# Kernel tuning notes

Measured on AMD Instinct MI355X. Metric: run time of the kernel, lower is better.

Reference implementation:

```python
import jax, jax.numpy as jnp
import numpy as np

NUM_CODES = 4096
TEMPERATURE = 1.0
EPS = 1e-08


def setup_inputs() -> dict:
    key = jax.random.key(0)
    k1, k2, k3 = jax.random.split(key, 3)
    B, D, T = 16, 512, 1500
    encoder_stride = 320
    student_features = jax.random.normal(k1, (B, D, T), dtype=jnp.float32)
    codebook = jax.random.normal(k2, (NUM_CODES, D), dtype=jnp.float32)
    lengths = jax.random.randint(k3, (B,), 0, T * encoder_stride, dtype=jnp.int64)
    return {
        "student_features": student_features,
        "codebook": codebook,
        "lengths": lengths,
        "encoder_stride": encoder_stride,
    }


def _length_mask(lengths, T, stride):
    # frame t is valid iff t < floor(length / stride)  -> (B, T) float mask
    n_valid = jnp.minimum(lengths // stride, T)
    return (jnp.arange(T)[None, :] < n_valid[:, None]).astype(jnp.float32)


def reference(student_features, codebook, lengths, encoder_stride):
    B, D, T = student_features.shape
    mask = _length_mask(lengths, T, encoder_stride)            # (B, T)
    z = jnp.transpose(student_features, (0, 2, 1)).reshape(-1, D)  # (N, D), N = B*T
    # Euclidean cdist via ||z||^2 + ||c||^2 - 2 z c^T (same as torch.cdist GEMM path)
    z2 = jnp.sum(z * z, axis=-1, keepdims=True)                # (N, 1)
    c2 = jnp.sum(codebook * codebook, axis=-1)                 # (K,)
    d2 = z2 + c2[None, :] - 2.0 * (z @ codebook.T)             # (N, K)
    distances = jnp.sqrt(jnp.maximum(d2, 1e-12))
    logits = -distances / TEMPERATURE
    probs = jax.nn.softmax(logits, axis=-1)                    # (N, K)
    probs_masked = probs * mask.reshape(-1, 1)
    code_dist = jnp.sum(probs_masked, axis=0)                  # (K,)
    code_dist = code_dist / (jnp.sum(code_dist) + EPS)
    entropy = -jnp.sum(code_dist * jnp.log(code_dist + EPS))
    max_entropy = jnp.log(jnp.float32(NUM_CODES))
    return 1.0 - entropy / max_entropy
```

## Files before the change

kernel.cpp:

```cpp
#include <hip/hip_runtime.h>
#include <hip/hip_bf16.h>

#define NUM_B   16
#define DIM     512
#define TT      1500
#define NROWS   (NUM_B * TT)
#define NCODES  4096
#define ROW_TILES ((NROWS + 127) / 128)
#define NROWS_PAD (ROW_TILES * 128)
#define NSLICE  8
#define SHIFTC  30.0f
#define NBLKX   (NCODES / 128)
#define TBLKS   (NUM_B * 47)
#define CBLKS   (NCODES / 4)
#define NZERO   (NROWS_PAD + NSLICE * NCODES)

typedef __bf16 bf16x8 __attribute__((ext_vector_type(8)));
typedef float  floatx4 __attribute__((ext_vector_type(4)));
typedef unsigned short ushortx8 __attribute__((ext_vector_type(8)));

__device__ __forceinline__ void glds16(const void* g, void* l) {
    __builtin_amdgcn_global_load_lds(
        (__attribute__((address_space(1))) void*)(void*)g,
        (__attribute__((address_space(3))) void*)l, 16, 0, 0);
}

__global__ __launch_bounds__(256) void k_prep(
    const float* __restrict__ sf, const float* __restrict__ cb,
    unsigned short* __restrict__ zbf, unsigned short* __restrict__ cbbf,
    float* __restrict__ z2, float* __restrict__ c2, float* __restrict__ zero0) {
    int id = blockIdx.x, tid = threadIdx.x;
    if (id < TBLKS) {
        __shared__ float tile[32][257];
        int b = id / 47, t0 = (id % 47) * 32;
        int tl = tid & 31, dg = tid >> 5;
        int tr = tid >> 3, dgr = tid & 7;
        int tg = t0 + tr;
        float ssq = 0.f;
        unsigned short* dst = zbf + (size_t)(b * TT + tg) * DIM;
#pragma unroll
        for (int half = 0; half < 2; ++half) {
            int dbase = half * 256;
            if (half) __syncthreads();
            int t = t0 + tl;
            if (t < TT) {
                const float* src = sf + (size_t)(b * DIM + dbase + dg * 32) * TT + t;
#pragma unroll
                for (int k = 0; k < 32; ++k)
                    tile[tl][dg * 32 + k] = src[(size_t)k * TT];
            }
            __syncthreads();
            if (tg < TT) {
#pragma unroll
                for (int seg = 0; seg < 4; ++seg) {
                    int d0 = seg * 64 + dgr * 8;
                    unsigned int h[8];
#pragma unroll
                    for (int i2 = 0; i2 < 8; ++i2) {
                        __hip_bfloat16 hb = __float2bfloat16(tile[tr][d0 + i2]);
                        h[i2] = __builtin_bit_cast(unsigned short, hb);
                        float vb = __bfloat162float(hb);
                        ssq += vb * vb;
                    }
                    uint4 o;
                    o.x = h[0] | (h[1] << 16); o.y = h[2] | (h[3] << 16);
                    o.z = h[4] | (h[5] << 16); o.w = h[6] | (h[7] << 16);
                    *(uint4*)(dst + dbase + d0) = o;
                }
            }
        }
        ssq += __shfl_xor(ssq, 1); ssq += __shfl_xor(ssq, 2); ssq += __shfl_xor(ssq, 4);
        if (dgr == 0 && tg < TT) z2[b * TT + tg] = ssq;
    } else {
        int ci = id - TBLKS;
        int gid = ci * 256 + tid;
        if (gid < NZERO) zero0[gid] = 0.f;
        int k = ci * 4 + (tid >> 6);
        int lane = tid & 63;
        const float4* src = (const float4*)(cb + (size_t)k * DIM + lane * 8);
        float4 a = src[0], b2 = src[1];
        float vals[8] = {a.x, a.y, a.z, a.w, b2.x, b2.y, b2.z, b2.w};
        float s = 0.f;
        unsigned int h[8];
#pragma unroll
        for (int i = 0; i < 8; ++i) {
            __hip_bfloat16 hb = __float2bfloat16(vals[i]);
            h[i] = __builtin_bit_cast(unsigned short, hb);
            float vb = __bfloat162float(hb);
            s += vb * vb;
        }
        uint4 o;
        o.x = h[0] | (h[1] << 16); o.y = h[2] | (h[3] << 16);
        o.z = h[4] | (h[5] << 16); o.w = h[6] | (h[7] << 16);
        *(uint4*)(cbbf + (size_t)k * DIM + lane * 8) = o;
#pragma unroll
        for (int off = 32; off >= 1; off >>= 1) s += __shfl_down(s, off);
        if (lane == 0) c2[k] = s;
    }
}

__global__ __launch_bounds__(256, 2) void k_gemm1(
    const unsigned short* __restrict__ zbf, const unsigned short* __restrict__ cbbf,
    const float* __restrict__ z2, const float* __restrict__ c2,
    const int* __restrict__ lengths, const int* __restrict__ stride_p,
    float* __restrict__ Sg, unsigned short* __restrict__ Eg) {
    __shared__ unsigned short As[128 * 64];
    __shared__ unsigned short Bs[128 * 64];
    __shared__ float z2s[128], c2s[128];
    __shared__ unsigned char vldp[128];
    __shared__ int s_any;
    int tid = threadIdx.x;
    int r0 = blockIdx.y * 128, c0 = blockIdx.x * 128;
    if (tid == 0) s_any = 0;
    __syncthreads();
    if (tid < 128) {
        int n = r0 + tid;
        int valid = 0;
        if (n < NROWS) {
            int b = n / TT, t = n - b * TT;
            int stride = stride_p[0];
            int nv = lengths[b] / stride;
            if (nv > TT) nv = TT;
            valid = (t < nv);
        }
        if (valid) atomicOr(&s_any, 1);
        vldp[tid] = (unsigned char)valid;
        z2s[tid] = z2[r0 + tid];
        c2s[tid] = c2[c0 + tid];
    }
    __syncthreads();
    if (!s_any) return;

    int wave = tid >> 6, lane = tid & 63;
    int l15 = lane & 15, l4 = lane >> 4;
    int wr = (wave >> 1) * 64, wc = (wave & 1) * 64;

    int srow = lane >> 3;
    int scg = (lane & 7) ^ srow;
    const unsigned short* ag = zbf + (size_t)(r0 + wave * 32 + srow) * DIM + scg * 8;
    const unsigned short* bg = cbbf + (size_t)(c0 + wave * 32 + srow) * DIM + scg * 8;
    unsigned short* al = As + (wave * 32) * 64;
    unsigned short* bl = Bs + (wave * 32) * 64;

    floatx4 acc[4][4];
    const floatx4 zero = {0.f, 0.f, 0.f, 0.f};
#pragma unroll
    for (int i = 0; i < 4; ++i)
#pragma unroll
        for (int j = 0; j < 4; ++j) acc[i][j] = zero;

    int sw = l15 & 7;

    for (int kc = 0; kc < 8; ++kc) {
#pragma unroll
        for (int q = 0; q < 4; ++q) {
            glds16(ag + (size_t)q * 8 * DIM + kc * 64, al + q * 8 * 64);
            glds16(bg + (size_t)q * 8 * DIM + kc * 64, bl + q * 8 * 64);
        }
        __syncthreads();
#pragma unroll
        for (int ks = 0; ks < 64; ks += 32) {
            int g = (ks >> 3) + l4;
            int pcg = g ^ sw;
            bf16x8 av[4], bv[4];
#pragma unroll
            for (int i = 0; i < 4; ++i)
                av[i] = __builtin_bit_cast(bf16x8,
                    *(const ushortx8*)&As[(wr + 16 * i + l15) * 64 + pcg * 8]);
#pragma unroll
            for (int j = 0; j < 4; ++j)
                bv[j] = __builtin_bit_cast(bf16x8,
                    *(const ushortx8*)&Bs[(wc + 16 * j + l15) * 64 + pcg * 8]);
#pragma unroll
            for (int i = 0; i < 4; ++i)
#pragma unroll
                for (int j = 0; j < 4; ++j)
                    acc[i][j] = __builtin_amdgcn_mfma_f32_16x16x32_bf16(av[i], bv[j], acc[i][j], 0, 0, 0);
        }
        __syncthreads();
    }

#pragma unroll
    for (int i = 0; i < 4; ++i) {
#pragma unroll
        for (int r = 0; r < 4; ++r) {
            int rl = wr + 16 * i + 4 * l4 + r;
            bool rv = vldp[rl] != 0;
            float z2v = z2s[rl];
            float s = 0.f;
            unsigned short* Ep = Eg + (size_t)(r0 + rl) * NCODES + c0 + wc + l15;
#pragma unroll
            for (int j = 0; j < 4; ++j) {
                int cl = wc + 16 * j + l15;
                float d2 = z2v + c2s[cl] - 2.0f * acc[i][j][r];
                float d = sqrtf(fmaxf(d2, 1e-12f));
                float e = __expf(SHIFTC - d);
                s += e;
                if (rv) Ep[16 * j] = __builtin_bit_cast(unsigned short, __float2bfloat16(e));
            }
            s += __shfl_xor(s, 1); s += __shfl_xor(s, 2);
            s += __shfl_xor(s, 4); s += __shfl_xor(s, 8);
            if (l15 == 0 && rv) atomicAdd(&Sg[r0 + rl], s);
        }
    }
}

__global__ __launch_bounds__(256) void k_scan(
    const unsigned short* __restrict__ Eg, const float* __restrict__ Sg,
    const int* __restrict__ lengths, const int* __restrict__ stride_p,
    float* __restrict__ cdp) {
    __shared__ float rs[32];
    __shared__ int s_any;
    int tid = threadIdx.x;
    int r0 = blockIdx.y * 32;
    if (tid == 0) s_any = 0;
    __syncthreads();
    if (tid < 32) {
        int n = r0 + tid;
        int valid = 0;
        if (n < NROWS) {
            int b = n / TT, t = n - b * TT;
            int nv = lengths[b] / stride_p[0];
            if (nv > TT) nv = TT;
            valid = (t < nv);
        }
        if (valid) atomicOr(&s_any, 1);
        rs[tid] = valid ? 1.0f / Sg[n] : 0.0f;
    }
    __syncthreads();
    if (!s_any) return;

    int col0 = blockIdx.x * 2048 + tid * 8;
    float acc[8] = {0.f, 0.f, 0.f, 0.f, 0.f, 0.f, 0.f, 0.f};
    for (int nn = 0; nn < 32; ++nn) {
        float rn = rs[nn];
        if (rn == 0.f) continue;
        uint4 v = *(const uint4*)(Eg + (size_t)(r0 + nn) * NCODES + col0);
        unsigned int u[4] = {v.x, v.y, v.z, v.w};
#pragma unroll
        for (int q = 0; q < 4; ++q) {
            acc[2 * q]     += rn * __builtin_bit_cast(float, u[q] << 16);
            acc[2 * q + 1] += rn * __builtin_bit_cast(float, u[q] & 0xffff0000u);
        }
    }
    float* outp = cdp + (size_t)(blockIdx.y & (NSLICE - 1)) * NCODES;
#pragma unroll
    for (int t = 0; t < 8; ++t) atomicAdd(&outp[col0 + t], acc[t]);
}

template <int PASS>
__global__ __launch_bounds__(256, 2) void k_gemm(
    const unsigned short* __restrict__ zbf, const unsigned short* __restrict__ cbbf,
    const float* __restrict__ z2, const float* __restrict__ c2,
    const int* __restrict__ lengths, const int* __restrict__ stride_p,
    float* __restrict__ Sg, float* __restrict__ cd) {
    __shared__ unsigned short As[128 * 64];
    __shared__ unsigned short Bs[128 * 64];
    __shared__ float z2s[128], c2s[128], rs[128];
    __shared__ int s_any;
    int tid = threadIdx.x;
    int r0 = blockIdx.y * 128, c0 = blockIdx.x * 128;
    if (tid == 0) s_any = 0;
    __syncthreads();
    if (tid < 128) {
        int n = r0 + tid;
        int valid = 0;
        if (n < NROWS) {
            int b = n / TT, t = n - b * TT;
            int stride = stride_p[0];
            int nv = lengths[b] / stride;
            if (nv > TT) nv = TT;
            valid = (t < nv);
        }
        if (valid) atomicOr(&s_any, 1);
        z2s[tid] = z2[r0 + tid];
        c2s[tid] = c2[c0 + tid];
        if (PASS == 2) rs[tid] = valid ? (1.0f / Sg[r0 + tid]) : 0.0f;
    }
    __syncthreads();
    if (!s_any) return;

    int wave = tid >> 6, lane = tid & 63;
    int l15 = lane & 15, l4 = lane >> 4;
    int wr = (wave >> 1) * 64, wc = (wave & 1) * 64;
    int srow = lane >> 3;
    int scg = (lane & 7) ^ srow;
    const unsigned short* ag = zbf + (size_t)(r0 + wave * 32 + srow) * DIM + scg * 8;
    const unsigned short* bg = cbbf + (size_t)(c0 + wave * 32 + srow) * DIM + scg * 8;
    unsigned short* al = As + (wave * 32) * 64;
    unsigned short* bl = Bs + (wave * 32) * 64;

    floatx4 acc[4][4];
    const floatx4 zero = {0.f, 0.f, 0.f, 0.f};
#pragma unroll
    for (int i = 0; i < 4; ++i)
#pragma unroll
        for (int j = 0; j < 4; ++j) acc[i][j] = zero;
    int sw = l15 & 7;
    for (int kc = 0; kc < 8; ++kc) {
#pragma unroll
        for (int q = 0; q < 4; ++q) {
            glds16(ag + (size_t)q * 8 * DIM + kc * 64, al + q * 8 * 64);
            glds16(bg + (size_t)q * 8 * DIM + kc * 64, bl + q * 8 * 64);
        }
        __syncthreads();
#pragma unroll
        for (int ks = 0; ks < 64; ks += 32) {
            int g = (ks >> 3) + l4;
            int pcg = g ^ sw;
            bf16x8 av[4], bv[4];
#pragma unroll
            for (int i = 0; i < 4; ++i)
                av[i] = __builtin_bit_cast(bf16x8, *(const ushortx8*)&As[(wr + 16 * i + l15) * 64 + pcg * 8]);
#pragma unroll
            for (int j = 0; j < 4; ++j)
                bv[j] = __builtin_bit_cast(bf16x8, *(const ushortx8*)&Bs[(wc + 16 * j + l15) * 64 + pcg * 8]);
#pragma unroll
            for (int i = 0; i < 4; ++i)
#pragma unroll
                for (int j = 0; j < 4; ++j)
                    acc[i][j] = __builtin_amdgcn_mfma_f32_16x16x32_bf16(av[i], bv[j], acc[i][j], 0, 0, 0);
        }
        __syncthreads();
    }
    if (PASS == 1) {
#pragma unroll
        for (int i = 0; i < 4; ++i) {
#pragma unroll
            for (int r = 0; r < 4; ++r) {
                int rl = wr + 16 * i + 4 * l4 + r;
                float z2v = z2s[rl];
                float s = 0.f;
#pragma unroll
                for (int j = 0; j < 4; ++j) {
                    int cl = wc + 16 * j + l15;
                    float d2 = z2v + c2s[cl] - 2.0f * acc[i][j][r];
                    float d = sqrtf(fmaxf(d2, 1e-12f));
                    s += __expf(SHIFTC - d);
                }
                s += __shfl_xor(s, 1); s += __shfl_xor(s, 2);
                s += __shfl_xor(s, 4); s += __shfl_xor(s, 8);
                if (l15 == 0) atomicAdd(&Sg[r0 + rl], s);
            }
        }
    } else {
#pragma unroll
        for (int j = 0; j < 4; ++j) {
            int cl = wc + 16 * j + l15;
            float c2v = c2s[cl];
            float cs = 0.f;
#pragma unroll
            for (int i = 0; i < 4; ++i) {
#pragma unroll
                for (int r = 0; r < 4; ++r) {
                    int rl = wr + 16 * i + 4 * l4 + r;
                    float d2 = z2s[rl] + c2v - 2.0f * acc[i][j][r];
                    float d = sqrtf(fmaxf(d2, 1e-12f));
                    cs += __expf(SHIFTC - d) * rs[rl];
                }
            }
            cs += __shfl_xor(cs, 16); cs += __shfl_xor(cs, 32);
            if (l4 == 0) atomicAdd(&cd[c0 + cl], cs);
        }
    }
}

__global__ __launch_bounds__(1024) void k_final(const float* __restrict__ cdp,
                                                float* __restrict__ out) {
    __shared__ float red[16];
    __shared__ float tot_s;
    int tid = threadIdx.x, lane = tid & 63, wave = tid >> 6;
    float vloc[4];
    float t = 0.f;
#pragma unroll
    for (int q = 0; q < 4; ++q) {
        int i = tid + q * 1024;
        float v = 0.f;
#pragma unroll
        for (int s = 0; s < NSLICE; ++s) v += cdp[(size_t)s * NCODES + i];
        vloc[q] = v;
        t += v;
    }
#pragma unroll
    for (int off = 32; off >= 1; off >>= 1) t += __shfl_down(t, off);
    if (lane == 0) red[wave] = t;
    __syncthreads();
    if (tid == 0) {
        float tt = 0.f;
#pragma unroll
        for (int w = 0; w < 16; ++w) tt += red[w];
        tot_s = tt;
    }
    __syncthreads();
    float inv = 1.0f / (tot_s + 1e-8f);
    float e = 0.f;
#pragma unroll
    for (int q = 0; q < 4; ++q) {
        float p = vloc[q] * inv;
        e += p * __logf(p + 1e-8f);
    }
#pragma unroll
    for (int off = 32; off >= 1; off >>= 1) e += __shfl_down(e, off);
    if (lane == 0) red[wave] = e;
    __syncthreads();
    if (tid == 0) {
        float ee = 0.f;
#pragma unroll
        for (int w = 0; w < 16; ++w) ee += red[w];
        out[0] = 1.0f - (-ee) / __logf((float)NCODES);
    }
}

extern "C" void kernel_launch(void* const* d_in, const int* in_sizes, int n_in,
                              void* d_out, int out_size, void* d_ws, size_t ws_size,
                              hipStream_t stream) {
    const float* sf = (const float*)d_in[0];
    const float* cb = (const float*)d_in[1];
    const int* lengths = (const int*)d_in[2];
    const int* stride_p = (const int*)d_in[3];

    float* wsf = (float*)d_ws;
    float* Sg = wsf;
    float* cdp = Sg + NROWS_PAD;
    const size_t OFF_Z2 = NZERO;
    const size_t OFF_C2 = OFF_Z2 + NROWS_PAD;
    const size_t OFF_ZB = (OFF_C2 + NCODES + 3) & ~(size_t)3;
    float* z2 = wsf + OFF_Z2;
    float* c2 = wsf + OFF_C2;
    unsigned short* zbf = (unsigned short*)(wsf + OFF_ZB);
    unsigned short* cbbf = zbf + (size_t)NROWS_PAD * DIM;
    unsigned short* Eg = cbbf + (size_t)NCODES * DIM;

    size_t need = OFF_ZB * 4
                + ((size_t)NROWS_PAD * DIM + (size_t)NCODES * DIM
                 + (size_t)NROWS_PAD * NCODES) * 2;

    k_prep<<<dim3(TBLKS + CBLKS), 256, 0, stream>>>(sf, cb, zbf, cbbf, z2, c2, Sg);
    if (ws_size >= need) {
        k_gemm1<<<dim3(NBLKX, ROW_TILES), 256, 0, stream>>>(
            zbf, cbbf, z2, c2, lengths, stride_p, Sg, Eg);
        k_scan<<<dim3(2, NROWS_PAD / 32), 256, 0, stream>>>(
            Eg, Sg, lengths, stride_p, cdp);
    } else {
        k_gemm<1><<<dim3(NBLKX, ROW_TILES), 256, 0, stream>>>(zbf, cbbf, z2, c2, lengths, stride_p, Sg, cdp);
        k_gemm<2><<<dim3(NBLKX, ROW_TILES), 256, 0, stream>>>(zbf, cbbf, z2, c2, lengths, stride_p, Sg, cdp);
    }
    k_final<<<1, 1024, 0, stream>>>(cdp, (float*)d_out);
}
```

Baseline: 238.9 us.

## Rewrite distance GEMM with 256x256 tiles and double-buffered software-pipelined LDS

Replaces the 128x128 single-buffered GEMM1 kernel with a 512-thread, 256x256-tile kernel. It double-buffers LDS and interleaves global-to-LDS staging of the next K tiles with MFMA phases, using hand-placed waitcnt and barriers, inline ds_read_b128 and s_setprio. It also swizzles the workgroup order for cache locality and reshapes the epilogue so each lane writes 4 contiguous bf16 values instead of scattered 2-byte stores. The aim is to hide load latency and cut per-tile overhead. The cost is 128KB of LDS per block, which limits occupancy to one block per CU, plus fragile manual synchronisation.

New measurement: 315.1 us. 1.32x slower.

```diff
diff --git a/kernel.cpp b/kernel.cpp
--- a/kernel.cpp
+++ b/kernel.cpp
@@ -15,6 +15,11 @@
 #define CBLKS   (NCODES / 4)
 #define NZERO   (NROWS_PAD + NSLICE * NCODES)
 
+#define NTY2 (NROWS_PAD / 256)
+#define NTX2 (NCODES / 256)
+#define NWG2 (NTY2 * NTX2)
+#define KTILES (DIM / 64)
+
 typedef __bf16 bf16x8 __attribute__((ext_vector_type(8)));
 typedef float  floatx4 __attribute__((ext_vector_type(4)));
 typedef unsigned short ushortx8 __attribute__((ext_vector_type(8)));
@@ -99,15 +104,256 @@
     }
 }
 
-__global__ __launch_bounds__(256, 2) void k_gemm1(
+
+#define DSR(dst, addr) asm volatile("ds_read_b128 %0, %1" : "=v"(dst) : "v"(addr))
+#define PIPE_SYNC() do { \
+    asm volatile("s_waitcnt vmcnt(8)" ::: "memory"); \
+    asm volatile("s_barrier" ::: "memory"); \
+    asm volatile("s_waitcnt lgkmcnt(0)" ::: "memory"); \
+    __builtin_amdgcn_sched_barrier(0); \
+} while (0)
+#define PIPE_POST() asm volatile("s_barrier" ::: "memory")
+
+#define STG_A(TT_, H_) do { \
+    const unsigned short* _s = agp + (size_t)(H_) * 128 * DIM + (TT_) * 64; \
+    unsigned short* _d = &As[(TT_) & 1][H_][0] + (wave << 9); \
+    glds16(_s, _d); glds16(_s + (size_t)64 * DIM, _d + 4096); \
+} while (0)
+#define STG_B(TT_, H_) do { \
+    const unsigned short* _s = bgp + (size_t)(H_) * 128 * DIM + (TT_) * 64; \
+    unsigned short* _d = &Bs[(TT_) & 1][H_][0] + (wave << 9); \
+    glds16(_s, _d); glds16(_s + (size_t)64 * DIM, _d + 4096); \
+} while (0)
+
+#define MFMA_PH(IB, NQ) do { \
+    __builtin_amdgcn_s_setprio(1); \
+    _Pragma("unroll") \
+    for (int ii = 0; ii < 4; ++ii) { \
+        _Pragma("unroll") \
+        for (int jj = 0; jj < 2; ++jj) { \
+            floatx4 c_ = acc[(IB) + ii][(NQ) * 2 + jj]; \
+            c_ = __builtin_amdgcn_mfma_f32_16x16x32_bf16( \
+                __builtin_bit_cast(bf16x8, bv[NQ][jj][0]), \
+                __builtin_bit_cast(bf16x8, av[ii][0]), c_, 0, 0, 0); \
+            c_ = __builtin_amdgcn_mfma_f32_16x16x32_bf16( \
+                __builtin_bit_cast(bf16x8, bv[NQ][jj][1]), \
+                __builtin_bit_cast(bf16x8, av[ii][1]), c_, 0, 0, 0); \
+            acc[(IB) + ii][(NQ) * 2 + jj] = c_; \
+        } \
+    } \
+    __builtin_amdgcn_s_setprio(0); \
+} while (0)
+
+__global__ __launch_bounds__(512, 2) void k_gemm1(
     const unsigned short* __restrict__ zbf, const unsigned short* __restrict__ cbbf,
     const float* __restrict__ z2, const float* __restrict__ c2,
     const int* __restrict__ lengths, const int* __restrict__ stride_p,
     float* __restrict__ Sg, unsigned short* __restrict__ Eg) {
-    __shared__ unsigned short As[128 * 64];
-    __shared__ unsigned short Bs[128 * 64];
-    __shared__ float z2s[128], c2s[128];
-    __shared__ unsigned char vldp[128];
+    __shared__ alignas(16) unsigned short As[2][2][8192];
+    __shared__ alignas(16) unsigned short Bs[2][2][8192];
+    __shared__ float z2s[256], c2s[256];
+    __shared__ unsigned char vldp[256];
+    __shared__ int s_any;
+
+    int tid = threadIdx.x;
+    int wg = blockIdx.x;
+    int swz = (wg & 7) * (NWG2 / 8) + (wg >> 3);
+    int bx = swz & (NTX2 - 1);
+    int by = swz >> 4;
+    int r0 = by * 256, c0 = bx * 256;
+
+    if (tid == 0) s_any = 0;
+    __syncthreads();
+    if (tid < 256) {
+        int n = r0 + tid;
+        int valid = 0;
+        if (n < NROWS) {
+            int b = n / TT, t_ = n - b * TT;
+            int nv = lengths[b] / stride_p[0];
+            if (nv > TT) nv = TT;
+            valid = (t_ < nv);
+        }
+        if (valid) atomicOr(&s_any, 1);
+        vldp[tid] = (unsigned char)valid;
+        z2s[tid] = z2[r0 + tid];
+        c2s[tid] = c2[c0 + tid];
+    }
+    __syncthreads();
+    if (!s_any) return;
+
+    int wave = tid >> 6, lane = tid & 63;
+    int l15 = lane & 15, l4 = lane >> 4;
+    int wr2 = wave >> 2;
+    int wc4 = wave & 3;
+
+    int srow8 = lane >> 3;
+    int sg = (lane & 7) ^ srow8;
+    const unsigned short* agp = zbf + (size_t)(r0 + wave * 8 + srow8) * DIM + sg * 8;
+    const unsigned short* bgp = cbbf + (size_t)(c0 + wave * 8 + srow8) * DIM + sg * 8;
+
+    unsigned AsB = (unsigned)(size_t)&As[0][0][0];
+    unsigned BsB = (unsigned)(size_t)&Bs[0][0][0];
+    unsigned rowA = (unsigned)((wr2 * 16 + l15) * 128);
+    unsigned rowB = (unsigned)((wc4 * 16 + l15) * 128);
+    unsigned p0 = (unsigned)(((l4) ^ (l15 & 7)) * 16);
+    unsigned p1 = (unsigned)(((4 + l4) ^ (l15 & 7)) * 16);
+
+    floatx4 acc[8][4];
+    const floatx4 zacc = {0.f, 0.f, 0.f, 0.f};
+#pragma unroll
+    for (int i = 0; i < 8; ++i)
+#pragma unroll
+        for (int j = 0; j < 4; ++j) acc[i][j] = zacc;
+
+    STG_A(0, 0); STG_B(0, 0); STG_B(0, 1); STG_A(0, 1); STG_A(1, 0); STG_B(1, 0);
+    asm volatile("s_waitcnt vmcnt(8)" ::: "memory");
+    asm volatile("s_barrier" ::: "memory");
+
+#pragma unroll
+    for (int t = 0; t < KTILES; ++t) {
+        unsigned dbase = (unsigned)((t & 1) * 32768);
+        unsigned aAh0 = AsB + dbase + rowA;
+        unsigned aAh1 = aAh0 + 16384u;
+        unsigned aBh0 = BsB + dbase + rowB;
+        unsigned aBh1 = aBh0 + 16384u;
+        ushortx8 av[4][2];
+        ushortx8 bv[2][2][2];
+
+        {
+            unsigned a0 = aAh0 + p0, a1 = aAh0 + p1;
+            DSR(av[0][0], a0); DSR(av[1][0], a0 + 4096u);
+            DSR(av[2][0], a0 + 8192u); DSR(av[3][0], a0 + 12288u);
+            DSR(av[0][1], a1); DSR(av[1][1], a1 + 4096u);
+            DSR(av[2][1], a1 + 8192u); DSR(av[3][1], a1 + 12288u);
+            unsigned b0 = aBh0 + p0, b1 = aBh0 + p1;
+            DSR(bv[0][0][0], b0); DSR(bv[0][1][0], b0 + 8192u);
+            DSR(bv[0][0][1], b1); DSR(bv[0][1][1], b1 + 8192u);
+        }
+        if (t + 1 < KTILES) STG_B(t + 1, 1);
+        PIPE_SYNC();
+        MFMA_PH(0, 0);
+        PIPE_POST();
+
+        {
+            unsigned b0 = aBh1 + p0, b1 = aBh1 + p1;
+            DSR(bv[1][0][0], b0); DSR(bv[1][1][0], b0 + 8192u);
+            DSR(bv[1][0][1], b1); DSR(bv[1][1][1], b1 + 8192u);
+        }
+        if (t + 1 < KTILES) STG_A(t + 1, 1);
+        PIPE_SYNC();
+        MFMA_PH(0, 1);
+        PIPE_POST();
+
+        {
+            unsigned a0 = aAh1 + p0, a1 = aAh1 + p1;
+            DSR(av[0][0], a0); DSR(av[1][0], a0 + 4096u);
+            DSR(av[2][0], a0 + 8192u); DSR(av[3][0], a0 + 12288u);
+            DSR(av[0][1], a1); DSR(av[1][1], a1 + 4096u);
+            DSR(av[2][1], a1 + 8192u); DSR(av[3][1], a1 + 12288u);
+        }
+        if (t + 2 < KTILES) STG_A(t + 2, 0);
+        PIPE_SYNC();
+        MFMA_PH(4, 0);
+        PIPE_POST();
+
+        if (t + 2 < KTILES) STG_B(t + 2, 0);
+        PIPE_SYNC();
+        MFMA_PH(4, 1);
+        PIPE_POST();
+    }
+
+    float c2r[4][4];
+#pragma unroll
+    for (int j = 0; j < 4; ++j)
+#pragma unroll
+        for (int r = 0; r < 4; ++r)
+            c2r[j][r] = c2s[j * 64 + wc4 * 16 + l4 * 4 + r];
+
+#pragma unroll
+    for (int i = 0; i < 8; ++i) {
+        int rl = i * 32 + wr2 * 16 + l15;
+        bool rv = vldp[rl] != 0;
+        float z2v = z2s[rl];
+        float s = 0.f;
+        unsigned short* Ep = Eg + (size_t)(r0 + rl) * NCODES + c0 + wc4 * 16 + l4 * 4;
+#pragma unroll
+        for (int j = 0; j < 4; ++j) {
+            float e[4];
+#pragma unroll
+            for (int r = 0; r < 4; ++r) {
+                float d2 = z2v + c2r[j][r] - 2.0f * acc[i][j][r];
+                float d = sqrtf(fmaxf(d2, 1e-12f));
+                e[r] = __expf(SHIFTC - d);
+                s += e[r];
+            }
+            if (rv) {
+                unsigned h0 = __builtin_bit_cast(unsigned short, __float2bfloat16(e[0]));
+                unsigned h1 = __builtin_bit_cast(unsigned short, __float2bfloat16(e[1]));
+                unsigned h2 = __builtin_bit_cast(unsigned short, __float2bfloat16(e[2]));
+                unsigned h3 = __builtin_bit_cast(unsigned short, __float2bfloat16(e[3]));
+                uint2 o;
+                o.x = h0 | (h1 << 16);
+                o.y = h2 | (h3 << 16);
+                *(uint2*)(Ep + (size_t)j * 64) = o;
+            }
+        }
+        s += __shfl_xor(s, 16); s += __shfl_xor(s, 32);
+        if (l4 == 0 && rv) atomicAdd(&Sg[r0 + rl], s);
+    }
+}
+
+__global__ __launch_bounds__(256) void k_scan(
+    const unsigned short* __restrict__ Eg, const float* __restrict__ Sg,
+    const int* __restrict__ lengths, const int* __restrict__ stride_p,
+    float* __restrict__ cdp) {
+    __shared__ float rs[32];
+    __shared__ int s_any;
+    int tid = threadIdx.x;
+    int r0 = blockIdx.y * 32;
+    if (tid == 0) s_any = 0;
+    __syncthreads();
+    if (tid < 32) {
+        int n = r0 + tid;
+        int valid = 0;
+        if (n < NROWS) {
+            int b = n / TT, t = n - b * TT;
+            int nv = lengths[b] / stride_p[0];
+            if (nv > TT) nv = TT;
+            valid = (t < nv);
+        }
+        if (valid) atomicOr(&s_any, 1);
+        rs[tid] = valid ? 1.0f / Sg[n] : 0.0f;
+    }
+    __syncthreads();
+    if (!s_any) return;
+
+    int col0 = blockIdx.x * 2048 + tid * 8;
+    float acc[8] = {0.f, 0.f, 0.f, 0.f, 0.f, 0.f, 0.f, 0.f};
+    for (int nn = 0; nn < 32; ++nn) {
+        float rn = rs[nn];
+        if (rn == 0.f) continue;
+        uint4 v = *(const uint4*)(Eg + (size_t)(r0 + nn) * NCODES + col0);
+        unsigned int u[4] = {v.x, v.y, v.z, v.w};
+#pragma unroll
+        for (int q = 0; q < 4; ++q) {
+            acc[2 * q]     += rn * __builtin_bit_cast(float, u[q] << 16);
+            acc[2 * q + 1] += rn * __builtin_bit_cast(float, u[q] & 0xffff0000u);
+        }
+    }
+    float* outp = cdp + (size_t)(blockIdx.y & (NSLICE - 1)) * NCODES;
+#pragma unroll
+    for (int t = 0; t < 8; ++t) atomicAdd(&outp[col0 + t], acc[t]);
+}
+
+template <int PASS>
+__global__ __launch_bounds__(256, 2) void k_gemm(
+    const unsigned short* __restrict__ zbf, const unsigned short* __restrict__ cbbf,
+    const float* __restrict__ z2, const float* __restrict__ c2,
+    const int* __restrict__ lengths, const int* __restrict__ stride_p,
+    float* __restrict__ Sg, float* __restrict__ cd) {
+    __shared__ unsigned short Asf[128 * 64];
+    __shared__ unsigned short Bsf[128 * 64];
+    __shared__ float z2s[128], c2s[128], rs[128];
     __shared__ int s_any;
     int tid = threadIdx.x;
     int r0 = blockIdx.y * 128, c0 = blockIdx.x * 128;
@@ -124,155 +370,6 @@
             valid = (t < nv);
         }
         if (valid) atomicOr(&s_any, 1);
-        vldp[tid] = (unsigned char)valid;
-        z2s[tid] = z2[r0 + tid];
-        c2s[tid] = c2[c0 + tid];
-    }
-    __syncthreads();
-    if (!s_any) return;
-
-    int wave = tid >> 6, lane = tid & 63;
-    int l15 = lane & 15, l4 = lane >> 4;
-    int wr = (wave >> 1) * 64, wc = (wave & 1) * 64;
-
-    int srow = lane >> 3;
-    int scg = (lane & 7) ^ srow;
-    const unsigned short* ag = zbf + (size_t)(r0 + wave * 32 + srow) * DIM + scg * 8;
-    const unsigned short* bg = cbbf + (size_t)(c0 + wave * 32 + srow) * DIM + scg * 8;
-    unsigned short* al = As + (wave * 32) * 64;
-    unsigned short* bl = Bs + (wave * 32) * 64;
-
-    floatx4 acc[4][4];
-    const floatx4 zero = {0.f, 0.f, 0.f, 0.f};
-#pragma unroll
-    for (int i = 0; i < 4; ++i)
-#pragma unroll
-        for (int j = 0; j < 4; ++j) acc[i][j] = zero;
-
-    int sw = l15 & 7;
-
-    for (int kc = 0; kc < 8; ++kc) {
-#pragma unroll
-        for (int q = 0; q < 4; ++q) {
-            glds16(ag + (size_t)q * 8 * DIM + kc * 64, al + q * 8 * 64);
-            glds16(bg + (size_t)q * 8 * DIM + kc * 64, bl + q * 8 * 64);
-        }
-        __syncthreads();
-#pragma unroll
-        for (int ks = 0; ks < 64; ks += 32) {
-            int g = (ks >> 3) + l4;
-            int pcg = g ^ sw;
-            bf16x8 av[4], bv[4];
-#pragma unroll
-            for (int i = 0; i < 4; ++i)
-                av[i] = __builtin_bit_cast(bf16x8,
-                    *(const ushortx8*)&As[(wr + 16 * i + l15) * 64 + pcg * 8]);
-#pragma unroll
-            for (int j = 0; j < 4; ++j)
-                bv[j] = __builtin_bit_cast(bf16x8,
-                    *(const ushortx8*)&Bs[(wc + 16 * j + l15) * 64 + pcg * 8]);
-#pragma unroll
-            for (int i = 0; i < 4; ++i)
-#pragma unroll
-                for (int j = 0; j < 4; ++j)
-                    acc[i][j] = __builtin_amdgcn_mfma_f32_16x16x32_bf16(av[i], bv[j], acc[i][j], 0, 0, 0);
-        }
-        __syncthreads();
-    }
-
-#pragma unroll
-    for (int i = 0; i < 4; ++i) {
-#pragma unroll
-        for (int r = 0; r < 4; ++r) {
-            int rl = wr + 16 * i + 4 * l4 + r;
-            bool rv = vldp[rl] != 0;
-            float z2v = z2s[rl];
-            float s = 0.f;
-            unsigned short* Ep = Eg + (size_t)(r0 + rl) * NCODES + c0 + wc + l15;
-#pragma unroll
-            for (int j = 0; j < 4; ++j) {
-                int cl = wc + 16 * j + l15;
-                float d2 = z2v + c2s[cl] - 2.0f * acc[i][j][r];
-                float d = sqrtf(fmaxf(d2, 1e-12f));
-                float e = __expf(SHIFTC - d);
-                s += e;
-                if (rv) Ep[16 * j] = __builtin_bit_cast(unsigned short, __float2bfloat16(e));
-            }
-            s += __shfl_xor(s, 1); s += __shfl_xor(s, 2);
-            s += __shfl_xor(s, 4); s += __shfl_xor(s, 8);
-            if (l15 == 0 && rv) atomicAdd(&Sg[r0 + rl], s);
-        }
-    }
-}
-
-__global__ __launch_bounds__(256) void k_scan(
-    const unsigned short* __restrict__ Eg, const float* __restrict__ Sg,
-    const int* __restrict__ lengths, const int* __restrict__ stride_p,
-    float* __restrict__ cdp) {
-    __shared__ float rs[32];
-    __shared__ int s_any;
-    int tid = threadIdx.x;
-    int r0 = blockIdx.y * 32;
-    if (tid == 0) s_any = 0;
-    __syncthreads();
-    if (tid < 32) {
-        int n = r0 + tid;
-        int valid = 0;
-        if (n < NROWS) {
-            int b = n / TT, t = n - b * TT;
-            int nv = lengths[b] / stride_p[0];
-            if (nv > TT) nv = TT;
-            valid = (t < nv);
-        }
-        if (valid) atomicOr(&s_any, 1);
-        rs[tid] = valid ? 1.0f / Sg[n] : 0.0f;
-    }
-    __syncthreads();
-    if (!s_any) return;
-
-    int col0 = blockIdx.x * 2048 + tid * 8;
-    float acc[8] = {0.f, 0.f, 0.f, 0.f, 0.f, 0.f, 0.f, 0.f};
-    for (int nn = 0; nn < 32; ++nn) {
-        float rn = rs[nn];
-        if (rn == 0.f) continue;
-        uint4 v = *(const uint4*)(Eg + (size_t)(r0 + nn) * NCODES + col0);
-        unsigned int u[4] = {v.x, v.y, v.z, v.w};
-#pragma unroll
-        for (int q = 0; q < 4; ++q) {
-            acc[2 * q]     += rn * __builtin_bit_cast(float, u[q] << 16);
-            acc[2 * q + 1] += rn * __builtin_bit_cast(float, u[q] & 0xffff0000u);
-        }
-    }
-    float* outp = cdp + (size_t)(blockIdx.y & (NSLICE - 1)) * NCODES;
-#pragma unroll
-    for (int t = 0; t < 8; ++t) atomicAdd(&outp[col0 + t], acc[t]);
-}
-
-template <int PASS>
-__global__ __launch_bounds__(256, 2) void k_gemm(
-    const unsigned short* __restrict__ zbf, const unsigned short* __restrict__ cbbf,
-    const float* __restrict__ z2, const float* __restrict__ c2,
-    const int* __restrict__ lengths, const int* __restrict__ stride_p,
-    float* __restrict__ Sg, float* __restrict__ cd) {
-    __shared__ unsigned short As[128 * 64];
-    __shared__ unsigned short Bs[128 * 64];
-    __shared__ float z2s[128], c2s[128], rs[128];
-    __shared__ int s_any;
-    int tid = threadIdx.x;
-    int r0 = blockIdx.y * 128, c0 = blockIdx.x * 128;
-    if (tid == 0) s_any = 0;
-    __syncthreads();
-    if (tid < 128) {
-        int n = r0 + tid;
-        int valid = 0;
-        if (n < NROWS) {
-            int b = n / TT, t = n - b * TT;
-            int stride = stride_p[0];
-            int nv = lengths[b] / stride;
-            if (nv > TT) nv = TT;
-            valid = (t < nv);
-        }
-        if (valid) atomicOr(&s_any, 1);
         z2s[tid] = z2[r0 + tid];
         c2s[tid] = c2[c0 + tid];
         if (PASS == 2) rs[tid] = valid ? (1.0f / Sg[r0 + tid]) : 0.0f;
@@ -287,8 +384,8 @@
     int scg = (lane & 7) ^ srow;
     const unsigned short* ag = zbf + (size_t)(r0 + wave * 32 + srow) * DIM + scg * 8;
     const unsigned short* bg = cbbf + (size_t)(c0 + wave * 32 + srow) * DIM + scg * 8;
-    unsigned short* al = As + (wave * 32) * 64;
-    unsigned short* bl = Bs + (wave * 32) * 64;
+    unsigned short* al = Asf + (wave * 32) * 64;
+    unsigned short* bl = Bsf + (wave * 32) * 64;
 
     floatx4 acc[4][4];
     const floatx4 zero = {0.f, 0.f, 0.f, 0.f};
@@ -308,18 +405,18 @@
         for (int ks = 0; ks < 64; ks += 32) {
             int g = (ks >> 3) + l4;
             int pcg = g ^ sw;
-            bf16x8 av[4], bv[4];
+            bf16x8 av[4], bvv[4];
 #pragma unroll
             for (int i = 0; i < 4; ++i)
-                av[i] = __builtin_bit_cast(bf16x8, *(const ushortx8*)&As[(wr + 16 * i + l15) * 64 + pcg * 8]);
+                av[i] = __builtin_bit_cast(bf16x8, *(const ushortx8*)&Asf[(wr + 16 * i + l15) * 64 + pcg * 8]);
 #pragma unroll
             for (int j = 0; j < 4; ++j)
-                bv[j] = __builtin_bit_cast(bf16x8, *(const ushortx8*)&Bs[(wc + 16 * j + l15) * 64 + pcg * 8]);
+                bvv[j] = __builtin_bit_cast(bf16x8, *(const ushortx8*)&Bsf[(wc + 16 * j + l15) * 64 + pcg * 8]);
 #pragma unroll
             for (int i = 0; i < 4; ++i)
 #pragma unroll
                 for (int j = 0; j < 4; ++j)
-                    acc[i][j] = __builtin_amdgcn_mfma_f32_16x16x32_bf16(av[i], bv[j], acc[i][j], 0, 0, 0);
+                    acc[i][j] = __builtin_amdgcn_mfma_f32_16x16x32_bf16(av[i], bvv[j], acc[i][j], 0, 0, 0);
         }
         __syncthreads();
     }
@@ -437,7 +534,7 @@
 
     k_prep<<<dim3(TBLKS + CBLKS), 256, 0, stream>>>(sf, cb, zbf, cbbf, z2, c2, Sg);
     if (ws_size >= need) {
-        k_gemm1<<<dim3(NBLKX, ROW_TILES), 256, 0, stream>>>(
+        k_gemm1<<<dim3(NWG2), 512, 0, stream>>>(
             zbf, cbbf, z2, c2, lengths, stride_p, Sg, Eg);
         k_scan<<<dim3(2, NROWS_PAD / 32), 256, 0, stream>>>(
             Eg, Sg, lengths, stride_p, cdp);
```
